# Kernel optimization log

Hardware: AMD Instinct MI355X
Metric: run time of the kernel (lower is better)

The kernel has to match this reference:

```python
import jax, jax.numpy as jnp
import numpy as np

B, N, D_IN, D_OUT = 4, 2048, 1024, 1024


def setup_inputs() -> dict:
    key = jax.random.key(0)
    k0, k1, k2, k3 = jax.random.split(key, 4)
    x = jax.random.normal(k0, (B, N, D_IN), dtype=jnp.float32)
    # torch Linear weight is [out, in]; store transposed [in, out] for x @ W
    W_query = jax.random.normal(k1, (D_IN, D_OUT), dtype=jnp.float32) * (D_IN ** -0.5)
    W_key = jax.random.normal(k2, (D_IN, D_OUT), dtype=jnp.float32) * (D_IN ** -0.5)
    W_value = jax.random.normal(k3, (D_IN, D_OUT), dtype=jnp.float32) * (D_IN ** -0.5)
    return {"x": x, "W_query": W_query, "W_key": W_key, "W_value": W_value}


def reference(x, W_query, W_key, W_value):
    # x: [B, N, D_IN]
    num_tokens = x.shape[1]
    embed_dim = x.shape[2]  # NB: original scales by INPUT embed dim
    q = jnp.einsum('bnd,de->bne', x, W_query)  # [B, N, D_OUT]
    k = jnp.einsum('bnd,de->bne', x, W_key)
    v = jnp.einsum('bnd,de->bne', x, W_value)
    scores = jnp.einsum('bqe,bke->bqk', q, k)  # [B, N, N]
    idx = jnp.arange(num_tokens)
    causal_mask = idx[None, :] > idx[:, None]  # True above diagonal
    scores = jnp.where(causal_mask[None, :, :], -jnp.inf, scores)
    scale = jnp.asarray(embed_dim, scores.dtype) ** 0.5
    attn = jax.nn.softmax(scores / scale, axis=-1)  # dropout p=0 (eval)
    context = jnp.einsum('bqk,bke->bqe', attn, v)  # [B, N, D_OUT]
    return context
```

## Files before the change

kernel.cpp:

```cpp
#include <hip/hip_runtime.h>


typedef __attribute__((ext_vector_type(8))) _Float16 half8;
typedef __attribute__((ext_vector_type(4))) _Float16 half4v;
typedef __attribute__((ext_vector_type(4))) float floatx4;

#define AS1 __attribute__((address_space(1)))
#define AS3 __attribute__((address_space(3)))

__device__ __forceinline__ void load16_lds(void* lds, const void* g) {
  __builtin_amdgcn_global_load_lds((AS1 void*)g, (AS3 void*)lds, 16, 0, 0);
}


__global__ __launch_bounds__(256)
void conv_f32_f16(const float* __restrict__ in, _Float16* __restrict__ out,
                  float* __restrict__ l) {
  if (blockIdx.x < 8192) {
    const int i = (blockIdx.x * 256 + threadIdx.x) << 2;
    float4 v = *(const float4*)(in + i);
    half4v o = { (_Float16)v.x, (_Float16)v.y, (_Float16)v.z, (_Float16)v.w };
    *(half4v*)(out + i) = o;
  } else {
    const int i = ((blockIdx.x - 8192) * 256 + threadIdx.x) << 2;
    *(float4*)(l + i) = float4{0.f, 0.f, 0.f, 0.f};
  }
}

__global__ __launch_bounds__(256)
void transpose_w(const float* __restrict__ W0, const float* __restrict__ W1,
                 const float* __restrict__ W2, _Float16* __restrict__ Wt) {
  const float* W = blockIdx.z == 0 ? W0 : (blockIdx.z == 1 ? W1 : W2);
  _Float16* out = Wt + (long long)blockIdx.z * 1048576;
  __shared__ _Float16 t[32][33];
  const int tx = threadIdx.x, ty = threadIdx.y;
  const int n0 = blockIdx.x << 5, k0 = blockIdx.y << 5;
#pragma unroll
  for (int i = 0; i < 4; ++i)
    t[ty + i * 8][tx] = (_Float16)W[(long long)(k0 + ty + i * 8) * 1024 + n0 + tx];
  __syncthreads();
#pragma unroll
  for (int i = 0; i < 4; ++i)
    out[(long long)(n0 + ty + i * 8) * 1024 + k0 + tx] = t[tx][ty + i * 8];
}

__global__ __launch_bounds__(256)
void gemm_qkv(const _Float16* __restrict__ A, const _Float16* __restrict__ B,
              _Float16* __restrict__ Q, _Float16* __restrict__ Kh,
              _Float16* __restrict__ Vt) {
  const int bm = blockIdx.y, bn = blockIdx.x;
  const _Float16* Ab = A + (long long)bm * 128 * 1024;
  const _Float16* Bb = B + (long long)bn * 128 * 1024;

  __shared__ _Float16 As[128][64];
  __shared__ _Float16 Bs[128][64];

  const int tid = threadIdx.x;
  const int wave = tid >> 6, lane = tid & 63;
  const int quad = lane >> 4, lr = lane & 15;
  const int wm = (wave >> 1) << 6, wn = (wave & 1) << 6;
  const int srow = lane >> 3;
  const int goff = ((lane & 7) ^ srow) << 3;

  floatx4 acc[4][4] = {};
  const _Float16* ga = Ab + (long long)(wave * 8 + srow) * 1024 + goff;
  const _Float16* gb = Bb + (long long)(wave * 8 + srow) * 1024 + goff;

  for (int k0 = 0; k0 < 1024; k0 += 64) {
    __syncthreads();
#pragma unroll
    for (int c = 0; c < 4; ++c) {
      load16_lds(&As[wave * 8 + 32 * c][0], ga + c * 32 * 1024);
      load16_lds(&Bs[wave * 8 + 32 * c][0], gb + c * 32 * 1024);
    }
    ga += 64; gb += 64;
    __syncthreads();

#pragma unroll
    for (int kk = 0; kk < 2; ++kk) {
      half8 af[4], bf[4];
#pragma unroll
      for (int i = 0; i < 4; ++i) {
        const int ra = wm + (i << 4) + lr;
        const int rb = wn + (i << 4) + lr;
        af[i] = *(const half8*)&As[ra][(((kk << 2) + quad) ^ (ra & 7)) << 3];
        bf[i] = *(const half8*)&Bs[rb][(((kk << 2) + quad) ^ (rb & 7)) << 3];
      }
#pragma unroll
      for (int i = 0; i < 4; ++i)
#pragma unroll
        for (int j = 0; j < 4; ++j)
          acc[i][j] = __builtin_amdgcn_mfma_f32_16x16x32_f16(af[i], bf[j], acc[i][j], 0, 0, 0);
    }
  }

  const int colb = bn * 128 + wn + lr;
  const int rowb = bm * 128 + wm + (quad << 2);

  if (bn < 16) {
    _Float16* C = (bn < 8) ? Q : Kh;
    const int cb = colb & 1023;
#pragma unroll
    for (int i = 0; i < 4; ++i)
#pragma unroll
      for (int j = 0; j < 4; ++j)
#pragma unroll
        for (int r = 0; r < 4; ++r)
          C[(long long)(rowb + (i << 4) + r) * 1024 + cb + (j << 4)] =
              (_Float16)acc[i][j][r];
  } else {
    const int b = rowb >> 11;
    const int tb = rowb & 2047;
#pragma unroll
    for (int i = 0; i < 4; ++i) {
      const int tok = tb + (i << 4);
#pragma unroll
      for (int j = 0; j < 4; ++j) {
        const int d = (colb & 1023) + (j << 4);
        half4v v = { (_Float16)acc[i][j][0], (_Float16)acc[i][j][1],
                     (_Float16)acc[i][j][2], (_Float16)acc[i][j][3] };
        *(half4v*)&Vt[(long long)b * 2097152 + (long long)d * 2048 + tok] = v;
      }
    }
  }
}

__global__ __launch_bounds__(256)
void gemm_s_exp(const _Float16* __restrict__ Q, const _Float16* __restrict__ Kh,
                _Float16* __restrict__ P, float* __restrict__ l) {
  int t = blockIdx.x;
  int bm = 0;
  for (;;) { const int c = bm + 1; if (t < c) break; t -= c; ++bm; }
  const int bn = t;
  const int bz = blockIdx.y;

  const _Float16* Ab = Q  + (long long)bz * 2097152 + (long long)bm * 128 * 1024;
  const _Float16* Bb = Kh + (long long)bz * 2097152 + (long long)bn * 128 * 1024;

  __shared__ _Float16 As[128][64];
  __shared__ _Float16 Bs[128][64];

  const int tid = threadIdx.x;
  const int wave = tid >> 6, lane = tid & 63;
  const int quad = lane >> 4, lr = lane & 15;
  const int wm = (wave >> 1) << 6, wn = (wave & 1) << 6;
  const int srow = lane >> 3;
  const int schunk = lane & 7;
  const int goff = (schunk ^ srow) << 3;

  floatx4 acc[4][4] = {};
  const _Float16* ga = Ab + (long long)(wave * 8 + srow) * 1024 + goff;
  const _Float16* gb = Bb + (long long)(wave * 8 + srow) * 1024 + goff;

  half8 pa[4], pb[4];
#pragma unroll
  for (int c = 0; c < 4; ++c) {
    pa[c] = *(const half8*)(ga + c * 32 * 1024);
    pb[c] = *(const half8*)(gb + c * 32 * 1024);
  }

  for (int it = 0; it < 16; ++it) {
    __syncthreads();
#pragma unroll
    for (int c = 0; c < 4; ++c) {
      *(half8*)&As[wave * 8 + 32 * c + srow][schunk << 3] = pa[c];
      *(half8*)&Bs[wave * 8 + 32 * c + srow][schunk << 3] = pb[c];
    }
    __syncthreads();
    if (it + 1 < 16) {
      const int k1 = (it + 1) << 6;
#pragma unroll
      for (int c = 0; c < 4; ++c) {
        pa[c] = *(const half8*)(ga + c * 32 * 1024 + k1);
        pb[c] = *(const half8*)(gb + c * 32 * 1024 + k1);
      }
    }

#pragma unroll
    for (int kk = 0; kk < 2; ++kk) {
      half8 af[4], bf[4];
#pragma unroll
      for (int i = 0; i < 4; ++i) {
        const int ra = wm + (i << 4) + lr;
        const int rb = wn + (i << 4) + lr;
        af[i] = *(const half8*)&As[ra][(((kk << 2) + quad) ^ (ra & 7)) << 3];
        bf[i] = *(const half8*)&Bs[rb][(((kk << 2) + quad) ^ (rb & 7)) << 3];
      }
#pragma unroll
      for (int i = 0; i < 4; ++i)
#pragma unroll
        for (int j = 0; j < 4; ++j)
          acc[i][j] = __builtin_amdgcn_mfma_f32_16x16x32_f16(af[i], bf[j], acc[i][j], 0, 0, 0);
    }
  }

  const int colb = bn * 128 + wn + lr;
  const int rowb = bm * 128 + wm + (quad << 2);
  _Float16* Pb = P + (long long)bz * 4194304;
  const float scl = 0.03125f;

  float rs[4][4];
#pragma unroll
  for (int i = 0; i < 4; ++i)
#pragma unroll
    for (int r = 0; r < 4; ++r) rs[i][r] = 0.f;

#pragma unroll
  for (int i = 0; i < 4; ++i)
#pragma unroll
    for (int j = 0; j < 4; ++j)
#pragma unroll
      for (int r = 0; r < 4; ++r) {
        const int q = rowb + (i << 4) + r;
        const int kcol = colb + (j << 4);
        const float pv = (kcol <= q) ? __expf(acc[i][j][r] * scl) : 0.f;
        Pb[(long long)q * 2048 + kcol] = (_Float16)pv;
        rs[i][r] += pv;
      }

#pragma unroll
  for (int i = 0; i < 4; ++i)
#pragma unroll
    for (int r = 0; r < 4; ++r) {
#pragma unroll
      for (int off = 1; off < 16; off <<= 1)
        rs[i][r] += __shfl_xor(rs[i][r], off);
    }
  if (lr == 0) {
    float* lb = l + bz * 2048;
#pragma unroll
    for (int i = 0; i < 4; ++i)
#pragma unroll
      for (int r = 0; r < 4; ++r)
        atomicAdd(&lb[rowb + (i << 4) + r], rs[i][r]);
  }
}

__global__ __launch_bounds__(256)
void gemm_pv(const _Float16* __restrict__ P, const _Float16* __restrict__ Vt,
             const float* __restrict__ l, float* __restrict__ out) {
  const int dn = blockIdx.x;
  const int bm = 15 - blockIdx.y;
  const int bz = blockIdx.z;
  const int niter = 2 * (bm + 1);

  const _Float16* Ab = P  + (long long)bz * 4194304 + (long long)bm * 128 * 2048;
  const _Float16* Bb = Vt + (long long)bz * 2097152 + (long long)dn * 128 * 2048;

  __shared__ _Float16 As[128][64];
  __shared__ _Float16 Bs[128][64];

  const int tid = threadIdx.x;
  const int wave = tid >> 6, lane = tid & 63;
  const int quad = lane >> 4, lr = lane & 15;
  const int wm = (wave >> 1) << 6, wn = (wave & 1) << 6;
  const int srow = lane >> 3;
  const int schunk = lane & 7;
  const int goff = (schunk ^ srow) << 3;

  floatx4 acc[4][4] = {};
  const _Float16* ga = Ab + (long long)(wave * 8 + srow) * 2048 + goff;
  const _Float16* gb = Bb + (long long)(wave * 8 + srow) * 2048 + goff;

  half8 pa[4], pb[4];
#pragma unroll
  for (int c = 0; c < 4; ++c) {
    pa[c] = *(const half8*)(ga + (long long)c * 32 * 2048);
    pb[c] = *(const half8*)(gb + (long long)c * 32 * 2048);
  }

  for (int it = 0; it < niter; ++it) {
    __syncthreads();
#pragma unroll
    for (int c = 0; c < 4; ++c) {
      *(half8*)&As[wave * 8 + 32 * c + srow][schunk << 3] = pa[c];
      *(half8*)&Bs[wave * 8 + 32 * c + srow][schunk << 3] = pb[c];
    }
    __syncthreads();
    if (it + 1 < niter) {
      const int k1 = (it + 1) << 6;
#pragma unroll
      for (int c = 0; c < 4; ++c) {
        pa[c] = *(const half8*)(ga + (long long)c * 32 * 2048 + k1);
        pb[c] = *(const half8*)(gb + (long long)c * 32 * 2048 + k1);
      }
    }

#pragma unroll
    for (int kk = 0; kk < 2; ++kk) {
      half8 af[4], bf[4];
#pragma unroll
      for (int i = 0; i < 4; ++i) {
        const int ra = wm + (i << 4) + lr;
        const int rb = wn + (i << 4) + lr;
        af[i] = *(const half8*)&As[ra][(((kk << 2) + quad) ^ (ra & 7)) << 3];
        bf[i] = *(const half8*)&Bs[rb][(((kk << 2) + quad) ^ (rb & 7)) << 3];
      }
#pragma unroll
      for (int i = 0; i < 4; ++i)
#pragma unroll
        for (int j = 0; j < 4; ++j)
          acc[i][j] = __builtin_amdgcn_mfma_f32_16x16x32_f16(af[i], bf[j], acc[i][j], 0, 0, 0);
    }
  }

  const int colb = dn * 128 + wn + lr;
  const int rowb = bm * 128 + wm + (quad << 2);
  const float* lb = l + bz * 2048;
  float* Cb = out + (long long)bz * 2097152;

  float linv[4][4];
#pragma unroll
  for (int i = 0; i < 4; ++i)
#pragma unroll
    for (int r = 0; r < 4; ++r)
      linv[i][r] = 1.0f / lb[rowb + (i << 4) + r];

#pragma unroll
  for (int i = 0; i < 4; ++i)
#pragma unroll
    for (int j = 0; j < 4; ++j)
#pragma unroll
      for (int r = 0; r < 4; ++r)
        Cb[(long long)(rowb + (i << 4) + r) * 1024 + colb + (j << 4)] =
            acc[i][j][r] * linv[i][r];
}


extern "C" void kernel_launch(void* const* d_in, const int* in_sizes, int n_in,
                              void* d_out, int out_size, void* d_ws, size_t ws_size,
                              hipStream_t stream) {
  const float* x  = (const float*)d_in[0];
  const float* Wq = (const float*)d_in[1];
  const float* Wk = (const float*)d_in[2];
  const float* Wv = (const float*)d_in[3];
  float* out = (float*)d_out;

  char* ws = (char*)d_ws;
  _Float16* xh = (_Float16*)(ws);
  _Float16* Wt = (_Float16*)(ws + 16777216);
  _Float16* Q  = (_Float16*)(ws + 23068672);
  _Float16* Kh = (_Float16*)(ws + 39845888);
  _Float16* Vt = (_Float16*)(ws + 56623104);
  _Float16* P  = (_Float16*)(ws + 73400320);
  float*    l  = (float*)   (ws + 106954752);

  conv_f32_f16<<<8200, 256, 0, stream>>>(x, xh, l);
  transpose_w<<<dim3(32, 32, 3), dim3(32, 8), 0, stream>>>(Wq, Wk, Wv, Wt);

  gemm_qkv<<<dim3(24, 64), 256, 0, stream>>>(xh, Wt, Q, Kh, Vt);

  gemm_s_exp<<<dim3(136, 4), 256, 0, stream>>>(Q, Kh, P, l);

  gemm_pv<<<dim3(8, 16, 4), 256, 0, stream>>>(P, Vt, l, out);
}
```

Measured before the change: 240.0 us.

## Rewrite QKV GEMM as 256x256 double-buffered, 8-wave pipelined kernel

The QKV projection GEMM now uses 256x256 output tiles with 512 threads, a double-buffered LDS ring fed by async global-to-LDS loads, and an explicitly scheduled loop. That loop interleaves LDS fragment reads, prefetch of the next k-tile and MFMA bursts under manual waitcnt, barriers and priority hints. A remapped 1D grid groups workgroups so that nearby ones share A and B tiles in cache. The aim is to hide global-load latency and raise MFMA utilisation, at the cost of 128KB of LDS (occupancy of one block per CU) and a fragile hand-written schedule.

After: 257.4 us. 1.07x slower.

```diff
diff --git a/kernel.cpp b/kernel.cpp
--- a/kernel.cpp
+++ b/kernel.cpp
@@ -44,84 +44,149 @@
     out[(long long)(n0 + ty + i * 8) * 1024 + k0 + tx] = t[tx][ty + i * 8];
 }
 
-__global__ __launch_bounds__(256)
+__global__ __launch_bounds__(512)
 void gemm_qkv(const _Float16* __restrict__ A, const _Float16* __restrict__ B,
               _Float16* __restrict__ Q, _Float16* __restrict__ Kh,
               _Float16* __restrict__ Vt) {
-  const int bm = blockIdx.y, bn = blockIdx.x;
-  const _Float16* Ab = A + (long long)bm * 128 * 1024;
-  const _Float16* Bb = B + (long long)bn * 128 * 1024;
-
-  __shared__ _Float16 As[128][64];
-  __shared__ _Float16 Bs[128][64];
+  const int wg = ((blockIdx.x & 7) * 48) + (blockIdx.x >> 3);
+  const int bm = wg / 12, bn = wg % 12;
+
+  const _Float16* Ab = A + (long long)bm * 256 * 1024;
+  const _Float16* Bb = B + (long long)bn * 256 * 1024;
+
+  __shared__ _Float16 As[2][256][64];
+  __shared__ _Float16 Bs[2][256][64];
 
   const int tid = threadIdx.x;
   const int wave = tid >> 6, lane = tid & 63;
   const int quad = lane >> 4, lr = lane & 15;
-  const int wm = (wave >> 1) << 6, wn = (wave & 1) << 6;
+  const int wm64 = (wave >> 2) << 6;
+  const int wn32 = (wave & 3) << 5;
   const int srow = lane >> 3;
   const int goff = ((lane & 7) ^ srow) << 3;
 
-  floatx4 acc[4][4] = {};
-  const _Float16* ga = Ab + (long long)(wave * 8 + srow) * 1024 + goff;
-  const _Float16* gb = Bb + (long long)(wave * 8 + srow) * 1024 + goff;
-
-  for (int k0 = 0; k0 < 1024; k0 += 64) {
-    __syncthreads();
-#pragma unroll
-    for (int c = 0; c < 4; ++c) {
-      load16_lds(&As[wave * 8 + 32 * c][0], ga + c * 32 * 1024);
-      load16_lds(&Bs[wave * 8 + 32 * c][0], gb + c * 32 * 1024);
-    }
-    ga += 64; gb += 64;
-    __syncthreads();
-
-#pragma unroll
-    for (int kk = 0; kk < 2; ++kk) {
-      half8 af[4], bf[4];
-#pragma unroll
-      for (int i = 0; i < 4; ++i) {
-        const int ra = wm + (i << 4) + lr;
-        const int rb = wn + (i << 4) + lr;
-        af[i] = *(const half8*)&As[ra][(((kk << 2) + quad) ^ (ra & 7)) << 3];
-        bf[i] = *(const half8*)&Bs[rb][(((kk << 2) + quad) ^ (rb & 7)) << 3];
-      }
-#pragma unroll
-      for (int i = 0; i < 4; ++i)
-#pragma unroll
-        for (int j = 0; j < 4; ++j)
-          acc[i][j] = __builtin_amdgcn_mfma_f32_16x16x32_f16(af[i], bf[j], acc[i][j], 0, 0, 0);
-    }
-  }
-
-  const int colb = bn * 128 + wn + lr;
-  const int rowb = bm * 128 + wm + (quad << 2);
-
-  if (bn < 16) {
-    _Float16* C = (bn < 8) ? Q : Kh;
-    const int cb = colb & 1023;
-#pragma unroll
-    for (int i = 0; i < 4; ++i)
-#pragma unroll
-      for (int j = 0; j < 4; ++j)
-#pragma unroll
-        for (int r = 0; r < 4; ++r)
-          C[(long long)(rowb + (i << 4) + r) * 1024 + cb + (j << 4)] =
-              (_Float16)acc[i][j][r];
+  const _Float16* gA = Ab + (long long)(wave * 8 + srow) * 1024 + goff;
+  const _Float16* gB = Bb + (long long)(wave * 8 + srow) * 1024 + goff;
+
+  floatx4 acc[2][4][2][2] = {};
+  half8 af[4][2], bf[2][2];
+
+#define STAGE_A(buf, half, kt)                                                \
+  load16_lds(&As[buf][(half) * 128 + wave * 8][0],                            \
+             gA + ((half) * 128) * 1024 + (kt) * 64);                         \
+  load16_lds(&As[buf][(half) * 128 + 64 + wave * 8][0],                       \
+             gA + ((half) * 128 + 64) * 1024 + (kt) * 64)
+
+#define STAGE_B(buf, half, kt)                                                \
+  load16_lds(&Bs[buf][(half) * 128 + wave * 8][0],                            \
+             gB + ((half) * 128) * 1024 + (kt) * 64);                         \
+  load16_lds(&Bs[buf][(half) * 128 + 64 + wave * 8][0],                       \
+             gB + ((half) * 128 + 64) * 1024 + (kt) * 64)
+
+#define DSR(buf, mh, nh)                                                      \
+  _Pragma("unroll") for (int ii = 0; ii < 4; ++ii) {                          \
+    const int ra = (mh) * 128 + wm64 + (ii << 4) + lr;                        \
+    af[ii][0] = *(const half8*)&As[buf][ra][((quad) ^ (ra & 7)) << 3];        \
+    af[ii][1] = *(const half8*)&As[buf][ra][((4 + quad) ^ (ra & 7)) << 3];    \
+  }                                                                           \
+  _Pragma("unroll") for (int jj = 0; jj < 2; ++jj) {                          \
+    const int rb = (nh) * 128 + wn32 + (jj << 4) + lr;                        \
+    bf[jj][0] = *(const half8*)&Bs[buf][rb][((quad) ^ (rb & 7)) << 3];        \
+    bf[jj][1] = *(const half8*)&Bs[buf][rb][((4 + quad) ^ (rb & 7)) << 3];    \
+  }
+
+#define MFMA8(mh, nh)                                                         \
+  __builtin_amdgcn_s_setprio(1);                                              \
+  _Pragma("unroll") for (int kk = 0; kk < 2; ++kk)                            \
+  _Pragma("unroll") for (int ii = 0; ii < 4; ++ii)                            \
+  _Pragma("unroll") for (int jj = 0; jj < 2; ++jj)                            \
+    acc[mh][ii][nh][jj] = __builtin_amdgcn_mfma_f32_16x16x32_f16(             \
+        af[ii][kk], bf[jj][kk], acc[mh][ii][nh][jj], 0, 0, 0);                \
+  __builtin_amdgcn_s_setprio(0)
+
+#define BAR() __builtin_amdgcn_s_barrier()
+#define LGKM0()                                                               \
+  do { asm volatile("s_waitcnt lgkmcnt(0)");                                  \
+       __builtin_amdgcn_sched_barrier(0); } while (0)
+#define VM4()                                                                 \
+  do { asm volatile("s_waitcnt vmcnt(4)");                                    \
+       __builtin_amdgcn_sched_barrier(0); } while (0)
+#define VM0()                                                                 \
+  do { asm volatile("s_waitcnt vmcnt(0)");                                    \
+       __builtin_amdgcn_sched_barrier(0); } while (0)
+
+  STAGE_A(0, 0, 0); STAGE_B(0, 0, 0); STAGE_A(0, 1, 0); STAGE_B(0, 1, 0);
+  STAGE_A(1, 0, 1); STAGE_B(1, 0, 1);
+  VM4();
+  BAR();
+
+  for (int i = 0; i < 7; ++i) {
+    const int t1 = 2 * i + 1, t2 = 2 * i + 2, t3 = 2 * i + 3;
+    DSR(0, 0, 0); STAGE_A(1, 1, t1); BAR(); LGKM0(); MFMA8(0, 0); BAR();
+    DSR(0, 0, 1); STAGE_B(1, 1, t1); BAR(); LGKM0(); MFMA8(0, 1); BAR();
+    DSR(0, 1, 0); STAGE_A(0, 0, t2); BAR(); LGKM0(); MFMA8(1, 0); BAR();
+    DSR(0, 1, 1); STAGE_B(0, 0, t2); BAR(); LGKM0(); MFMA8(1, 1); VM4(); BAR();
+    DSR(1, 0, 0); STAGE_A(0, 1, t2); BAR(); LGKM0(); MFMA8(0, 0); BAR();
+    DSR(1, 0, 1); STAGE_B(0, 1, t2); BAR(); LGKM0(); MFMA8(0, 1); BAR();
+    DSR(1, 1, 0); STAGE_A(1, 0, t3); BAR(); LGKM0(); MFMA8(1, 0); BAR();
+    DSR(1, 1, 1); STAGE_B(1, 0, t3); BAR(); LGKM0(); MFMA8(1, 1); VM4(); BAR();
+  }
+
+  DSR(0, 0, 0); STAGE_A(1, 1, 15); BAR(); LGKM0(); MFMA8(0, 0); BAR();
+  DSR(0, 0, 1); STAGE_B(1, 1, 15); BAR(); LGKM0(); MFMA8(0, 1); BAR();
+  DSR(0, 1, 0);                    BAR(); LGKM0(); MFMA8(1, 0); BAR();
+  DSR(0, 1, 1);                    BAR(); LGKM0(); MFMA8(1, 1); VM0(); BAR();
+  DSR(1, 0, 0);                    BAR(); LGKM0(); MFMA8(0, 0); BAR();
+  DSR(1, 0, 1);                    BAR(); LGKM0(); MFMA8(0, 1); BAR();
+  DSR(1, 1, 0);                    BAR(); LGKM0(); MFMA8(1, 0); BAR();
+  DSR(1, 1, 1);                    BAR(); LGKM0(); MFMA8(1, 1);
+
+#undef STAGE_A
+#undef STAGE_B
+#undef DSR
+#undef MFMA8
+#undef BAR
+#undef LGKM0
+#undef VM4
+#undef VM0
+
+  const int rb0 = bm * 256 + wm64 + (quad << 2);
+  const int cb0 = bn * 256 + wn32 + lr;
+
+  if (bn < 8) {
+    _Float16* C = (bn < 4) ? Q : Kh;
+#pragma unroll
+    for (int mh = 0; mh < 2; ++mh)
+#pragma unroll
+      for (int ii = 0; ii < 4; ++ii)
+#pragma unroll
+        for (int nh = 0; nh < 2; ++nh)
+#pragma unroll
+          for (int jj = 0; jj < 2; ++jj)
+#pragma unroll
+            for (int r = 0; r < 4; ++r)
+              C[(long long)(rb0 + mh * 128 + ii * 16 + r) * 1024 +
+                (((cb0 + nh * 128 + jj * 16)) & 1023)] =
+                  (_Float16)acc[mh][ii][nh][jj][r];
   } else {
-    const int b = rowb >> 11;
-    const int tb = rowb & 2047;
-#pragma unroll
-    for (int i = 0; i < 4; ++i) {
-      const int tok = tb + (i << 4);
-#pragma unroll
-      for (int j = 0; j < 4; ++j) {
-        const int d = (colb & 1023) + (j << 4);
-        half4v v = { (_Float16)acc[i][j][0], (_Float16)acc[i][j][1],
-                     (_Float16)acc[i][j][2], (_Float16)acc[i][j][3] };
-        *(half4v*)&Vt[(long long)b * 2097152 + (long long)d * 2048 + tok] = v;
-      }
-    }
+#pragma unroll
+    for (int mh = 0; mh < 2; ++mh)
+#pragma unroll
+      for (int ii = 0; ii < 4; ++ii) {
+        const int row = rb0 + mh * 128 + ii * 16;
+        const int b = row >> 11, tok = row & 2047;
+#pragma unroll
+        for (int nh = 0; nh < 2; ++nh)
+#pragma unroll
+          for (int jj = 0; jj < 2; ++jj) {
+            const int d = (cb0 - 2048) + nh * 128 + jj * 16;
+            half4v v = { (_Float16)acc[mh][ii][nh][jj][0],
+                         (_Float16)acc[mh][ii][nh][jj][1],
+                         (_Float16)acc[mh][ii][nh][jj][2],
+                         (_Float16)acc[mh][ii][nh][jj][3] };
+            *(half4v*)&Vt[(long long)b * 2097152 + (long long)d * 2048 + tok] = v;
+          }
+      }
   }
 }
 
@@ -348,7 +413,7 @@
   conv_f32_f16<<<8200, 256, 0, stream>>>(x, xh, l);
   transpose_w<<<dim3(32, 32, 3), dim3(32, 8), 0, stream>>>(Wq, Wk, Wv, Wt);
 
-  gemm_qkv<<<dim3(24, 64), 256, 0, stream>>>(xh, Wt, Q, Kh, Vt);
+  gemm_qkv<<<dim3(384), 512, 0, stream>>>(xh, Wt, Q, Kh, Vt);
 
   gemm_s_exp<<<dim3(136, 4), 256, 0, stream>>>(Q, Kh, P, l);
 
```

## Rewrite QKV GEMM as 256x192 tile with double-buffered LDS ping-pong pipeline

Applied to the files above, without the earlier changes.

The QKV projection GEMM now uses 512-thread blocks computing 256x192 output tiles, down from 128x128. LDS is double-buffered and global-to-LDS loads for the next k-tile are interleaved with MFMA groups under explicit waitcnt and barriers. MFMA groups run at raised s_setprio, and the 512 blocks are swizzled across the grid for L2 locality. The goal is to hide load latency and raise data reuse per block. The cost is more registers and LDS per block, and a hand-scheduled pipeline that is fragile.

After: 239.2 us. About the same (-0.4%).

```diff
diff --git a/kernel.cpp b/kernel.cpp
--- a/kernel.cpp
+++ b/kernel.cpp
@@ -44,85 +44,148 @@
     out[(long long)(n0 + ty + i * 8) * 1024 + k0 + tx] = t[tx][ty + i * 8];
 }
 
-__global__ __launch_bounds__(256)
+__global__ __launch_bounds__(512)
 void gemm_qkv(const _Float16* __restrict__ A, const _Float16* __restrict__ B,
               _Float16* __restrict__ Q, _Float16* __restrict__ Kh,
               _Float16* __restrict__ Vt) {
-  const int bm = blockIdx.y, bn = blockIdx.x;
-  const _Float16* Ab = A + (long long)bm * 128 * 1024;
-  const _Float16* Bb = B + (long long)bn * 128 * 1024;
-
-  __shared__ _Float16 As[128][64];
-  __shared__ _Float16 Bs[128][64];
+  const int wg = ((blockIdx.x & 7) << 6) + (blockIdx.x >> 3);
+  const int bm = wg >> 4, bn = wg & 15;
+
+  const _Float16* Ab = A + (long long)bm * 256 * 1024;
+  const _Float16* Bb = B + (long long)bn * 192 * 1024;
+
+  __shared__ _Float16 As[2][256][64];
+  __shared__ _Float16 Bs[2][192][64];
 
   const int tid = threadIdx.x;
   const int wave = tid >> 6, lane = tid & 63;
   const int quad = lane >> 4, lr = lane & 15;
-  const int wm = (wave >> 1) << 6, wn = (wave & 1) << 6;
+  const int rowb = (wave >> 2) << 7;
+  const int colb = (wave & 3) * 48;
   const int srow = lane >> 3;
   const int goff = ((lane & 7) ^ srow) << 3;
 
-  floatx4 acc[4][4] = {};
-  const _Float16* ga = Ab + (long long)(wave * 8 + srow) * 1024 + goff;
-  const _Float16* gb = Bb + (long long)(wave * 8 + srow) * 1024 + goff;
-
-  for (int k0 = 0; k0 < 1024; k0 += 64) {
-    __syncthreads();
-#pragma unroll
-    for (int c = 0; c < 4; ++c) {
-      load16_lds(&As[wave * 8 + 32 * c][0], ga + c * 32 * 1024);
-      load16_lds(&Bs[wave * 8 + 32 * c][0], gb + c * 32 * 1024);
-    }
-    ga += 64; gb += 64;
-    __syncthreads();
-
-#pragma unroll
-    for (int kk = 0; kk < 2; ++kk) {
-      half8 af[4], bf[4];
-#pragma unroll
-      for (int i = 0; i < 4; ++i) {
-        const int ra = wm + (i << 4) + lr;
-        const int rb = wn + (i << 4) + lr;
-        af[i] = *(const half8*)&As[ra][(((kk << 2) + quad) ^ (ra & 7)) << 3];
-        bf[i] = *(const half8*)&Bs[rb][(((kk << 2) + quad) ^ (rb & 7)) << 3];
-      }
-#pragma unroll
-      for (int i = 0; i < 4; ++i)
-#pragma unroll
-        for (int j = 0; j < 4; ++j)
-          acc[i][j] = __builtin_amdgcn_mfma_f32_16x16x32_f16(af[i], bf[j], acc[i][j], 0, 0, 0);
-    }
-  }
-
-  const int colb = bn * 128 + wn + lr;
-  const int rowb = bm * 128 + wm + (quad << 2);
-
-  if (bn < 16) {
-    _Float16* C = (bn < 8) ? Q : Kh;
-    const int cb = colb & 1023;
-#pragma unroll
-    for (int i = 0; i < 4; ++i)
-#pragma unroll
-      for (int j = 0; j < 4; ++j)
-#pragma unroll
-        for (int r = 0; r < 4; ++r)
-          C[(long long)(rowb + (i << 4) + r) * 1024 + cb + (j << 4)] =
-              (_Float16)acc[i][j][r];
-  } else {
-    const int b = rowb >> 11;
-    const int tb = rowb & 2047;
-#pragma unroll
-    for (int i = 0; i < 4; ++i) {
-      const int tok = tb + (i << 4);
-#pragma unroll
-      for (int j = 0; j < 4; ++j) {
-        const int d = (colb & 1023) + (j << 4);
-        half4v v = { (_Float16)acc[i][j][0], (_Float16)acc[i][j][1],
-                     (_Float16)acc[i][j][2], (_Float16)acc[i][j][3] };
-        *(half4v*)&Vt[(long long)b * 2097152 + (long long)d * 2048 + tok] = v;
-      }
-    }
-  }
+  const _Float16* gA = Ab + (long long)srow * 1024 + goff;
+  const _Float16* gB = Bb + (long long)srow * 1024 + goff;
+
+  int arow[2][2], brow[3];
+#pragma unroll
+  for (int c = 0; c < 2; ++c) {
+    const int li = wave * 16 + c * 8;
+    const int r0 = (li < 64) ? li : li + 64;
+    arow[0][c] = r0;
+    arow[1][c] = r0 + 64;
+  }
+#pragma unroll
+  for (int c = 0; c < 3; ++c) brow[c] = wave * 24 + c * 8;
+
+  floatx4 acc[2][4][3] = {};
+  half8 af[4], bf[2][3];
+
+#define STAGE_A(buf, mh, kt)                                                  \
+  _Pragma("unroll") for (int c = 0; c < 2; ++c)                               \
+    load16_lds(&As[buf][arow[mh][c]][0],                                      \
+               gA + (long long)arow[mh][c] * 1024 + (long long)(kt) * 64)
+
+#define STAGE_B(buf, kt)                                                      \
+  _Pragma("unroll") for (int c = 0; c < 3; ++c)                               \
+    load16_lds(&Bs[buf][brow[c]][0],                                          \
+               gB + (long long)brow[c] * 1024 + (long long)(kt) * 64)
+
+#define DSRA(buf, mh, kk)                                                     \
+  _Pragma("unroll") for (int ii = 0; ii < 4; ++ii) {                          \
+    const int ra = rowb + (mh) * 64 + (ii << 4) + lr;                         \
+    af[ii] = *(const half8*)&As[buf][ra][((((kk) << 2) + quad) ^ (ra & 7)) << 3]; \
+  }
+
+#define DSRB(buf, kk)                                                         \
+  _Pragma("unroll") for (int jj = 0; jj < 3; ++jj) {                          \
+    const int rb = colb + (jj << 4) + lr;                                     \
+    bf[kk][jj] = *(const half8*)&Bs[buf][rb][((((kk) << 2) + quad) ^ (rb & 7)) << 3]; \
+  }
+
+#define MFMA12(mh, kk)                                                        \
+  __builtin_amdgcn_s_setprio(1);                                              \
+  _Pragma("unroll") for (int ii = 0; ii < 4; ++ii)                            \
+  _Pragma("unroll") for (int jj = 0; jj < 3; ++jj)                            \
+    acc[mh][ii][jj] = __builtin_amdgcn_mfma_f32_16x16x32_f16(                 \
+        af[ii], bf[kk][jj], acc[mh][ii][jj], 0, 0, 0);                        \
+  __builtin_amdgcn_s_setprio(0)
+
+#define BAR() __builtin_amdgcn_s_barrier()
+#define LGKM0()                                                               \
+  do { asm volatile("s_waitcnt lgkmcnt(0)");                                  \
+       __builtin_amdgcn_sched_barrier(0); } while (0)
+#define VM2()                                                                 \
+  do { asm volatile("s_waitcnt vmcnt(2)");                                    \
+       __builtin_amdgcn_sched_barrier(0); } while (0)
+#define VM0()                                                                 \
+  do { asm volatile("s_waitcnt vmcnt(0)");                                    \
+       __builtin_amdgcn_sched_barrier(0); } while (0)
+
+  STAGE_A(0, 0, 0); STAGE_A(0, 1, 0); STAGE_B(0, 0);
+  STAGE_A(1, 0, 1);
+  VM2();
+  BAR();
+
+  for (int i = 0; i < 7; ++i) {
+    const int t1 = 2 * i + 1, t2 = 2 * i + 2, t3 = 2 * i + 3;
+    DSRA(0,0,0); DSRB(0,0); STAGE_A(1,1,t1); BAR(); LGKM0(); MFMA12(0,0); BAR();
+    DSRA(0,0,1); DSRB(0,1); STAGE_B(1,t1);   BAR(); LGKM0(); MFMA12(0,1); BAR();
+    DSRA(0,1,1);            STAGE_A(0,0,t2); BAR(); LGKM0(); MFMA12(1,1); BAR();
+    DSRA(0,1,0);                             BAR(); LGKM0(); MFMA12(1,0); VM2(); BAR();
+    DSRA(1,0,0); DSRB(1,0); STAGE_A(0,1,t2); BAR(); LGKM0(); MFMA12(0,0); BAR();
+    DSRA(1,0,1); DSRB(1,1); STAGE_B(0,t2);   BAR(); LGKM0(); MFMA12(0,1); BAR();
+    DSRA(1,1,1);            STAGE_A(1,0,t3); BAR(); LGKM0(); MFMA12(1,1); BAR();
+    DSRA(1,1,0);                             BAR(); LGKM0(); MFMA12(1,0); VM2(); BAR();
+  }
+
+  DSRA(0,0,0); DSRB(0,0); STAGE_A(1,1,15); BAR(); LGKM0(); MFMA12(0,0); BAR();
+  DSRA(0,0,1); DSRB(0,1); STAGE_B(1,15);   BAR(); LGKM0(); MFMA12(0,1); BAR();
+  DSRA(0,1,1);                             BAR(); LGKM0(); MFMA12(1,1); BAR();
+  DSRA(0,1,0);                             BAR(); LGKM0(); MFMA12(1,0); VM0(); BAR();
+  DSRA(1,0,0); DSRB(1,0);                  BAR(); LGKM0(); MFMA12(0,0); BAR();
+  DSRA(1,0,1); DSRB(1,1);                  BAR(); LGKM0(); MFMA12(0,1); BAR();
+  DSRA(1,1,1);                             BAR(); LGKM0(); MFMA12(1,1); BAR();
+  DSRA(1,1,0);                             BAR(); LGKM0(); MFMA12(1,0);
+
+#undef STAGE_A
+#undef STAGE_B
+#undef DSRA
+#undef DSRB
+#undef MFMA12
+#undef BAR
+#undef LGKM0
+#undef VM2
+#undef VM0
+
+  const int row0 = bm * 256 + rowb + (quad << 2);
+  const int col0 = bn * 192 + colb + lr;
+
+#pragma unroll
+  for (int mh = 0; mh < 2; ++mh)
+#pragma unroll
+    for (int ii = 0; ii < 4; ++ii) {
+      const int row = row0 + mh * 64 + ii * 16;
+#pragma unroll
+      for (int jj = 0; jj < 3; ++jj) {
+        const int cseg = (bn * 192 + colb + jj * 16) >> 10;
+        const int col = col0 + jj * 16;
+        if (cseg < 2) {
+          _Float16* C = (cseg == 0) ? Q : Kh;
+          const int cc = col & 1023;
+#pragma unroll
+          for (int r = 0; r < 4; ++r)
+            C[(long long)(row + r) * 1024 + cc] = (_Float16)acc[mh][ii][jj][r];
+        } else {
+          const int b = row >> 11, tok = row & 2047;
+          const int d = col & 1023;
+          half4v v = { (_Float16)acc[mh][ii][jj][0], (_Float16)acc[mh][ii][jj][1],
+                       (_Float16)acc[mh][ii][jj][2], (_Float16)acc[mh][ii][jj][3] };
+          *(half4v*)&Vt[(long long)b * 2097152 + (long long)d * 2048 + tok] = v;
+        }
+      }
+    }
 }
 
 __global__ __launch_bounds__(256)
@@ -348,7 +411,7 @@
   conv_f32_f16<<<8200, 256, 0, stream>>>(x, xh, l);
   transpose_w<<<dim3(32, 32, 3), dim3(32, 8), 0, stream>>>(Wq, Wk, Wv, Wt);
 
-  gemm_qkv<<<dim3(24, 64), 256, 0, stream>>>(xh, Wt, Q, Kh, Vt);
+  gemm_qkv<<<dim3(512), 512, 0, stream>>>(xh, Wt, Q, Kh, Vt);
 
   gemm_s_exp<<<dim3(136, 4), 256, 0, stream>>>(Q, Kh, P, l);
 
```
